# Kernel optimization log

Hardware: AMD Instinct MI355X
Metric: run time of the kernel (lower is better)

Reference implementation:

```python
import jax, jax.numpy as jnp
import numpy as np

VOCAB = 267735
CUTOFFS = [0, 20000, 40000, 200000, 267735]
D_EMBED = 1024
D_PROJ = 1024
DIV_VAL = 4
EMB_SCALE = float(D_PROJ) ** 0.5


def setup_inputs() -> dict:
    key = jax.random.key(0)
    ks = jax.random.split(key, 9)
    input_ids = jax.random.randint(ks[0], (8, 2048), 0, VOCAB, dtype=jnp.int64)
    inp = {"input_ids": input_ids}
    for i in range(4):
        l, r = CUTOFFS[i], CUTOFFS[i + 1]
        d_i = D_EMBED // (DIV_VAL ** i)
        inp[f"emb{i}"] = jax.random.normal(ks[1 + 2 * i], (r - l, d_i), dtype=jnp.float32) * 0.02
        inp[f"proj{i}"] = jax.random.normal(ks[2 + 2 * i], (D_PROJ, d_i), dtype=jnp.float32) * 0.02
    return inp


def reference(input_ids, emb0, emb1, emb2, emb3, proj0, proj1, proj2, proj3):
    tables = [emb0, emb1, emb2, emb3]
    projs = [proj0, proj1, proj2, proj3]
    out = jnp.zeros(input_ids.shape + (D_PROJ,), dtype=jnp.float32)
    for i in range(4):
        l, r = CUTOFFS[i], CUTOFFS[i + 1]
        mask = (input_ids >= l) & (input_ids < r)                     # [B,S]
        idx = jnp.clip(input_ids - l, 0, r - l - 1)                   # [B,S]
        emb_i = tables[i][idx]                                        # [B,S,d_i]
        proj_i = jnp.einsum('bse,de->bsd', emb_i, projs[i])           # [B,S,D]
        out = out + jnp.where(mask[..., None], proj_i, 0.0)
    return out * EMB_SCALE
```

## Files before the change

### kernel.cpp

```cpp
#include <hip/hip_runtime.h>


constexpr int NTOK  = 16384;
constexpr int DPROJ = 1024;
constexpr float EMB_SCALE = 32.0f;
constexpr int SLOTX = 264;

typedef __attribute__((ext_vector_type(8))) short short8;
typedef __attribute__((ext_vector_type(4))) float float4v;

__global__ __launch_bounds__(256) void partition_kernel(
    const int* __restrict__ ids, int* __restrict__ cnt, int* __restrict__ lists)
{
    int t = blockIdx.x * 256 + threadIdx.x;
    int id = ids[t];
    int c = (id >= 200000) ? 3 : (id >= 40000) ? 2 : (id >= 20000) ? 1 : 0;
    int lane = threadIdx.x & 63;
    unsigned long long lt = (1ull << lane) - 1ull;
    int pos = 0;
#pragma unroll
    for (int i = 0; i < 4; ++i) {
        unsigned long long m = __ballot(c == i);
        int b = 0;
        if (lane == 0 && m) b = atomicAdd(&cnt[i], (int)__popcll(m));
        b = __shfl(b, 0);
        if (c == i) pos = b + (int)__popcll(m & lt);
    }
    lists[c * NTOK + pos] = t;
}

__device__ __forceinline__ void gload_lds16(const float* g, void* l) {
    __builtin_amdgcn_global_load_lds(
        (const __attribute__((address_space(1))) void*)g,
        (__attribute__((address_space(3))) void*)l, 16, 0, 0);
}

__device__ __forceinline__ short f2bf(float f) {
    unsigned u = __builtin_bit_cast(unsigned, f);
    u += 0x7FFFu + ((u >> 16) & 1u);
    return (short)(u >> 16);
}

__device__ __forceinline__ short8 cvt8f(float4 a, float4 b) {
    short8 r = { f2bf(a.x), f2bf(a.y), f2bf(a.z), f2bf(a.w),
                 f2bf(b.x), f2bf(b.y), f2bf(b.z), f2bf(b.w) };
    return r;
}

template<int D, int NC>
__device__ __forceinline__ void gemm_pipe(
    const int* __restrict__ ids, const float* __restrict__ emb,
    const float* __restrict__ proj, const int* __restrict__ list,
    int count, int lo, int mtile, int n0,
    float* __restrict__ out, char* smem, int* smTok, int* smRow)
{
    const int m0 = mtile * 64;
    if (m0 >= count) return;
    const int tid = threadIdx.x, lane = tid & 63, wv = tid >> 6;
    const int col = lane & 15, quad = lane >> 4;
    const int wr = (wv >> 1) * 32, wc = (wv & 1) * 32;

    if (tid < 64) {
        int m = m0 + tid;
        int tok = (m < count) ? list[m] : -1;
        smTok[tid] = tok;
        smRow[tid] = (tok >= 0) ? (ids[tok] - lo) : 0;
    }
    __syncthreads();

    float (*As)[2048] = (float(*)[2048])smem;
    float (*Bs)[2048] = (float(*)[2048])(smem + 2 * 8192);

    const float* srcA[2]; const float* srcB[2]; int LL[2];
#pragma unroll
    for (int i = 0; i < 2; ++i) {
        int L = i * 4096 + wv * 1024 + lane * 16;
        int row = L >> 7;
        int kblk = ((L >> 4) & 7) ^ (row & 7);
        LL[i] = L;
        srcA[i] = emb  + (size_t)smRow[row] * D + kblk * 4;
        srcB[i] = proj + (size_t)(n0 + row) * D + kblk * 4;
    }

    auto issue = [&](int c, int buf) {
        const int co = c * 32;
#pragma unroll
        for (int i = 0; i < 2; ++i) gload_lds16(srcA[i] + co, (char*)As[buf] + LL[i]);
#pragma unroll
        for (int i = 0; i < 2; ++i) gload_lds16(srcB[i] + co, (char*)Bs[buf] + LL[i]);
    };

    float4v acc[2][2] = {};
    auto compute = [&](int buf) {
        short8 af[2], bf[2];
#pragma unroll
        for (int m = 0; m < 2; ++m) {
            int row = wr + m * 16 + col;
            const float* Ab = As[buf] + row * 32;
            float4 x = *(const float4*)(Ab + (((2 * quad + 0) ^ (row & 7)) << 2));
            float4 y = *(const float4*)(Ab + (((2 * quad + 1) ^ (row & 7)) << 2));
            af[m] = cvt8f(x, y);
        }
#pragma unroll
        for (int n = 0; n < 2; ++n) {
            int row = wc + n * 16 + col;
            const float* Bb = Bs[buf] + row * 32;
            float4 x = *(const float4*)(Bb + (((2 * quad + 0) ^ (row & 7)) << 2));
            float4 y = *(const float4*)(Bb + (((2 * quad + 1) ^ (row & 7)) << 2));
            bf[n] = cvt8f(x, y);
        }
#pragma unroll
        for (int m = 0; m < 2; ++m)
#pragma unroll
            for (int n = 0; n < 2; ++n)
                acc[m][n] = __builtin_amdgcn_mfma_f32_16x16x32_bf16(
                    af[m], bf[n], acc[m][n], 0, 0, 0);
    };

    issue(0, 0);
    __syncthreads();
#pragma unroll
    for (int k = 0; k < NC; ++k) {
        if (k + 1 < NC) issue(k + 1, (k + 1) & 1);
        compute(k & 1);
        __syncthreads();
    }

#pragma unroll
    for (int m = 0; m < 2; ++m) {
#pragma unroll
        for (int r = 0; r < 4; ++r) {
            int tok = smTok[wr + m * 16 + quad * 4 + r];
            if (tok < 0) continue;
            float* op = out + (size_t)tok * DPROJ + n0 + wc + col;
            op[0]  = acc[m][0][r] * EMB_SCALE;
            op[16] = acc[m][1][r] * EMB_SCALE;
        }
    }
}

__device__ __forceinline__ void gemm_c3(
    const int* __restrict__ ids, const float* __restrict__ emb,
    const float* __restrict__ proj, const int* __restrict__ list,
    int count, int mtile, int n0,
    float* __restrict__ out, char* smem, int* smTok, int* smRow)
{
    const int m0 = mtile * 64;
    if (m0 >= count) return;
    const int tid = threadIdx.x, lane = tid & 63, wv = tid >> 6;
    const int col = lane & 15, quad = lane >> 4;
    const int wr = (wv >> 1) * 32, wc = (wv & 1) * 32;
    short (*Asm)[24] = (short(*)[24])smem;
    short (*Bsm)[24] = (short(*)[24])(smem + 64 * 24 * 2);

    if (tid < 64) {
        int m = m0 + tid;
        int tok = (m < count) ? list[m] : -1;
        smTok[tid] = tok;
        smRow[tid] = (tok >= 0) ? (ids[tok] - 200000) : 0;
    }
    __syncthreads();

    if (tid < 128) {
        int r = tid >> 1, c0 = (tid & 1) * 8;
        const float* p = emb + (size_t)smRow[r] * 16 + c0;
        float4 x = *(const float4*)p, y = *(const float4*)(p + 4);
        *(short8*)&Asm[r][c0] = cvt8f(x, y);
    } else {
        int t = tid - 128, r = t >> 1, c0 = (t & 1) * 8;
        const float* p = proj + (size_t)(n0 + r) * 16 + c0;
        float4 x = *(const float4*)p, y = *(const float4*)(p + 4);
        *(short8*)&Bsm[r][c0] = cvt8f(x, y);
    }
    __syncthreads();

    short8 z8 = {};
    short8 af[2], bf[2];
#pragma unroll
    for (int m = 0; m < 2; ++m)
        af[m] = (quad < 2) ? *(const short8*)&Asm[wr + m * 16 + col][quad * 8] : z8;
#pragma unroll
    for (int n = 0; n < 2; ++n)
        bf[n] = (quad < 2) ? *(const short8*)&Bsm[wc + n * 16 + col][quad * 8] : z8;

    float4v acc[2][2] = {};
#pragma unroll
    for (int m = 0; m < 2; ++m)
#pragma unroll
        for (int n = 0; n < 2; ++n)
            acc[m][n] = __builtin_amdgcn_mfma_f32_16x16x32_bf16(
                af[m], bf[n], acc[m][n], 0, 0, 0);

#pragma unroll
    for (int m = 0; m < 2; ++m) {
#pragma unroll
        for (int r = 0; r < 4; ++r) {
            int tok = smTok[wr + m * 16 + quad * 4 + r];
            if (tok < 0) continue;
            float* op = out + (size_t)tok * DPROJ + n0 + wc + col;
            op[0]  = acc[m][0][r] * EMB_SCALE;
            op[16] = acc[m][1][r] * EMB_SCALE;
        }
    }
}

__global__ __launch_bounds__(256) void adaptive_emb_gemm(
    const int* __restrict__ ids,
    const float* __restrict__ e0, const float* __restrict__ p0,
    const float* __restrict__ e1, const float* __restrict__ p1,
    const float* __restrict__ e2, const float* __restrict__ p2,
    const float* __restrict__ e3, const float* __restrict__ p3,
    const int* __restrict__ cnt, const int* __restrict__ lists,
    float* __restrict__ out)
{
    __shared__ __align__(16) char smem[32768];
    __shared__ int smTok[64], smRow[64];

    const int n0 = blockIdx.y * 64;
    int c0t = (cnt[0] + 63) >> 6;
    int c1t = (cnt[1] + 63) >> 6;
    int c2t = (cnt[2] + 63) >> 6;
    int c3t = (cnt[3] + 63) >> 6;
    int s = blockIdx.x;
    if (s < c0t) {
        gemm_pipe<1024, 32>(ids, e0, p0, lists, cnt[0], 0,
                            s, n0, out, smem, smTok, smRow);
        return;
    }
    s -= c0t;
    if (s < c1t) {
        gemm_pipe<256, 8>(ids, e1, p1, lists + NTOK, cnt[1], 20000,
                          s, n0, out, smem, smTok, smRow);
        return;
    }
    s -= c1t;
    if (s < c2t) {
        gemm_pipe<64, 2>(ids, e2, p2, lists + 2 * NTOK, cnt[2], 40000,
                         s, n0, out, smem, smTok, smRow);
        return;
    }
    s -= c2t;
    if (s < c3t)
        gemm_c3(ids, e3, p3, lists + 3 * NTOK, cnt[3], s, n0, out, smem, smTok, smRow);
}

extern "C" void kernel_launch(void* const* d_in, const int* in_sizes, int n_in,
                              void* d_out, int out_size, void* d_ws, size_t ws_size,
                              hipStream_t stream) {
    const int*   ids = (const int*)d_in[0];
    const float* e0  = (const float*)d_in[1];
    const float* p0  = (const float*)d_in[2];
    const float* e1  = (const float*)d_in[3];
    const float* p1  = (const float*)d_in[4];
    const float* e2  = (const float*)d_in[5];
    const float* p2  = (const float*)d_in[6];
    const float* e3  = (const float*)d_in[7];
    const float* p3  = (const float*)d_in[8];
    float* out = (float*)d_out;

    int* cnt   = (int*)d_ws;
    int* lists = cnt + 4;

    (void)hipMemsetAsync(cnt, 0, 4 * sizeof(int), stream);
    partition_kernel<<<dim3(NTOK / 256), 256, 0, stream>>>(ids, cnt, lists);

    adaptive_emb_gemm<<<dim3(SLOTX, DPROJ / 64), 256, 0, stream>>>(
        ids, e0, p0, e1, p1, e2, p2, e3, p3, cnt, lists, out);
}
```

Baseline: 235.1 us.

## Enlarge GEMM tiles to 128x128 and unify last cluster into pipelined path

Each block now covers a 128-token by 128-column tile instead of 64x64. Each wave computes all 128 rows against its own 32 columns, which raises reuse of the staged B tile and cuts the number of blocks and the redundant re-reads of the embedding and projection tiles. The dedicated cluster-3 kernel is removed in favour of a D=16 instance of the pipelined GEMM that zero-pads the unused K lanes. The cost is twice the LDS (64 KB per block), more accumulator registers, fewer blocks in flight, and token ids re-read from global memory in the epilogue.

```diff
diff --git a/kernel.cpp b/kernel.cpp
--- a/kernel.cpp
+++ b/kernel.cpp
@@ -4,7 +4,7 @@
 constexpr int NTOK  = 16384;
 constexpr int DPROJ = 1024;
 constexpr float EMB_SCALE = 32.0f;
-constexpr int SLOTX = 264;
+constexpr int SLOTX = 136;
 
 typedef __attribute__((ext_vector_type(8))) short short8;
 typedef __attribute__((ext_vector_type(4))) float float4v;
@@ -52,74 +52,80 @@
     const int* __restrict__ ids, const float* __restrict__ emb,
     const float* __restrict__ proj, const int* __restrict__ list,
     int count, int lo, int mtile, int n0,
-    float* __restrict__ out, char* smem, int* smTok, int* smRow)
+    float* __restrict__ out, char* smem)
 {
-    const int m0 = mtile * 64;
+    const int m0 = mtile * 128;
     if (m0 >= count) return;
     const int tid = threadIdx.x, lane = tid & 63, wv = tid >> 6;
     const int col = lane & 15, quad = lane >> 4;
-    const int wr = (wv >> 1) * 32, wc = (wv & 1) * 32;
-
-    if (tid < 64) {
+
+    int* tmp = (int*)smem;
+    if (tid < 128) {
         int m = m0 + tid;
-        int tok = (m < count) ? list[m] : -1;
-        smTok[tid] = tok;
-        smRow[tid] = (tok >= 0) ? (ids[tok] - lo) : 0;
+        int tok = (m < count) ? list[m] : 0;
+        tmp[tid] = (m < count) ? (ids[tok] - lo) : 0;
     }
     __syncthreads();
 
-    float (*As)[2048] = (float(*)[2048])smem;
-    float (*Bs)[2048] = (float(*)[2048])(smem + 2 * 8192);
-
-    const float* srcA[2]; const float* srcB[2]; int LL[2];
-#pragma unroll
-    for (int i = 0; i < 2; ++i) {
-        int L = i * 4096 + wv * 1024 + lane * 16;
+    int LL[4], rowA[4];
+#pragma unroll
+    for (int i = 0; i < 4; ++i) {
+        LL[i] = i * 4096 + wv * 1024 + lane * 16;
+        rowA[i] = tmp[LL[i] >> 7];
+    }
+    __syncthreads();
+
+    float (*As)[4096] = (float(*)[4096])smem;
+    float (*Bs)[4096] = (float(*)[4096])(smem + 2 * 16384);
+
+    const float* srcA[4]; const float* srcB[4];
+#pragma unroll
+    for (int i = 0; i < 4; ++i) {
+        int L = LL[i];
         int row = L >> 7;
-        int kblk = ((L >> 4) & 7) ^ (row & 7);
-        LL[i] = L;
-        srcA[i] = emb  + (size_t)smRow[row] * D + kblk * 4;
-        srcB[i] = proj + (size_t)(n0 + row) * D + kblk * 4;
+        int kb = ((L >> 4) & 7) ^ (row & 7);
+        int ka = (D >= 32 || kb * 4 < D) ? kb * 4 : 0;
+        srcA[i] = emb  + (size_t)rowA[i] * D + ka;
+        srcB[i] = proj + (size_t)(n0 + row) * D + ka;
     }
 
     auto issue = [&](int c, int buf) {
         const int co = c * 32;
 #pragma unroll
-        for (int i = 0; i < 2; ++i) gload_lds16(srcA[i] + co, (char*)As[buf] + LL[i]);
-#pragma unroll
-        for (int i = 0; i < 2; ++i) gload_lds16(srcB[i] + co, (char*)Bs[buf] + LL[i]);
+        for (int i = 0; i < 4; ++i) gload_lds16(srcA[i] + co, (char*)As[buf] + LL[i]);
+#pragma unroll
+        for (int i = 0; i < 4; ++i) gload_lds16(srcB[i] + co, (char*)Bs[buf] + LL[i]);
     };
 
-    float4v acc[2][2] = {};
+    float4v acc[8][2] = {};
     auto compute = [&](int buf) {
-        short8 af[2], bf[2];
-#pragma unroll
-        for (int m = 0; m < 2; ++m) {
-            int row = wr + m * 16 + col;
+        short8 bf[2];
+#pragma unroll
+        for (int n = 0; n < 2; ++n) {
+            int row = wv * 32 + n * 16 + col;
+            const float* Bb = Bs[buf] + row * 32;
+            float4 x = *(const float4*)(Bb + (((2 * quad + 0) ^ (row & 7)) << 2));
+            float4 y = *(const float4*)(Bb + (((2 * quad + 1) ^ (row & 7)) << 2));
+            if (D == 16 && quad >= 2) { x = float4{}; y = float4{}; }
+            bf[n] = cvt8f(x, y);
+        }
+#pragma unroll
+        for (int m = 0; m < 8; ++m) {
+            int row = m * 16 + col;
             const float* Ab = As[buf] + row * 32;
             float4 x = *(const float4*)(Ab + (((2 * quad + 0) ^ (row & 7)) << 2));
             float4 y = *(const float4*)(Ab + (((2 * quad + 1) ^ (row & 7)) << 2));
-            af[m] = cvt8f(x, y);
-        }
-#pragma unroll
-        for (int n = 0; n < 2; ++n) {
-            int row = wc + n * 16 + col;
-            const float* Bb = Bs[buf] + row * 32;
-            float4 x = *(const float4*)(Bb + (((2 * quad + 0) ^ (row & 7)) << 2));
-            float4 y = *(const float4*)(Bb + (((2 * quad + 1) ^ (row & 7)) << 2));
-            bf[n] = cvt8f(x, y);
-        }
-#pragma unroll
-        for (int m = 0; m < 2; ++m)
+            short8 af = cvt8f(x, y);
 #pragma unroll
             for (int n = 0; n < 2; ++n)
                 acc[m][n] = __builtin_amdgcn_mfma_f32_16x16x32_bf16(
-                    af[m], bf[n], acc[m][n], 0, 0, 0);
+                    af, bf[n], acc[m][n], 0, 0, 0);
+        }
     };
 
     issue(0, 0);
     __syncthreads();
-#pragma unroll
+#pragma unroll 2
     for (int k = 0; k < NC; ++k) {
         if (k + 1 < NC) issue(k + 1, (k + 1) & 1);
         compute(k & 1);
@@ -127,77 +133,13 @@
     }
 
 #pragma unroll
-    for (int m = 0; m < 2; ++m) {
+    for (int m = 0; m < 8; ++m) {
 #pragma unroll
         for (int r = 0; r < 4; ++r) {
-            int tok = smTok[wr + m * 16 + quad * 4 + r];
-            if (tok < 0) continue;
-            float* op = out + (size_t)tok * DPROJ + n0 + wc + col;
-            op[0]  = acc[m][0][r] * EMB_SCALE;
-            op[16] = acc[m][1][r] * EMB_SCALE;
-        }
-    }
-}
-
-__device__ __forceinline__ void gemm_c3(
-    const int* __restrict__ ids, const float* __restrict__ emb,
-    const float* __restrict__ proj, const int* __restrict__ list,
-    int count, int mtile, int n0,
-    float* __restrict__ out, char* smem, int* smTok, int* smRow)
-{
-    const int m0 = mtile * 64;
-    if (m0 >= count) return;
-    const int tid = threadIdx.x, lane = tid & 63, wv = tid >> 6;
-    const int col = lane & 15, quad = lane >> 4;
-    const int wr = (wv >> 1) * 32, wc = (wv & 1) * 32;
-    short (*Asm)[24] = (short(*)[24])smem;
-    short (*Bsm)[24] = (short(*)[24])(smem + 64 * 24 * 2);
-
-    if (tid < 64) {
-        int m = m0 + tid;
-        int tok = (m < count) ? list[m] : -1;
-        smTok[tid] = tok;
-        smRow[tid] = (tok >= 0) ? (ids[tok] - 200000) : 0;
-    }
-    __syncthreads();
-
-    if (tid < 128) {
-        int r = tid >> 1, c0 = (tid & 1) * 8;
-        const float* p = emb + (size_t)smRow[r] * 16 + c0;
-        float4 x = *(const float4*)p, y = *(const float4*)(p + 4);
-        *(short8*)&Asm[r][c0] = cvt8f(x, y);
-    } else {
-        int t = tid - 128, r = t >> 1, c0 = (t & 1) * 8;
-        const float* p = proj + (size_t)(n0 + r) * 16 + c0;
-        float4 x = *(const float4*)p, y = *(const float4*)(p + 4);
-        *(short8*)&Bsm[r][c0] = cvt8f(x, y);
-    }
-    __syncthreads();
-
-    short8 z8 = {};
-    short8 af[2], bf[2];
-#pragma unroll
-    for (int m = 0; m < 2; ++m)
-        af[m] = (quad < 2) ? *(const short8*)&Asm[wr + m * 16 + col][quad * 8] : z8;
-#pragma unroll
-    for (int n = 0; n < 2; ++n)
-        bf[n] = (quad < 2) ? *(const short8*)&Bsm[wc + n * 16 + col][quad * 8] : z8;
-
-    float4v acc[2][2] = {};
-#pragma unroll
-    for (int m = 0; m < 2; ++m)
-#pragma unroll
-        for (int n = 0; n < 2; ++n)
-            acc[m][n] = __builtin_amdgcn_mfma_f32_16x16x32_bf16(
-                af[m], bf[n], acc[m][n], 0, 0, 0);
-
-#pragma unroll
-    for (int m = 0; m < 2; ++m) {
-#pragma unroll
-        for (int r = 0; r < 4; ++r) {
-            int tok = smTok[wr + m * 16 + quad * 4 + r];
-            if (tok < 0) continue;
-            float* op = out + (size_t)tok * DPROJ + n0 + wc + col;
+            int mm = m * 16 + quad * 4 + r;
+            if (m0 + mm >= count) continue;
+            int tok = list[m0 + mm];
+            float* op = out + (size_t)tok * DPROJ + n0 + wv * 32 + col;
             op[0]  = acc[m][0][r] * EMB_SCALE;
             op[16] = acc[m][1][r] * EMB_SCALE;
         }
@@ -213,35 +155,31 @@
     const int* __restrict__ cnt, const int* __restrict__ lists,
     float* __restrict__ out)
 {
-    __shared__ __align__(16) char smem[32768];
-    __shared__ int smTok[64], smRow[64];
-
-    const int n0 = blockIdx.y * 64;
-    int c0t = (cnt[0] + 63) >> 6;
-    int c1t = (cnt[1] + 63) >> 6;
-    int c2t = (cnt[2] + 63) >> 6;
-    int c3t = (cnt[3] + 63) >> 6;
+    __shared__ __align__(16) char smem[65536];
+
+    const int n0 = blockIdx.y * 128;
+    int c0t = (cnt[0] + 127) >> 7;
+    int c1t = (cnt[1] + 127) >> 7;
+    int c2t = (cnt[2] + 127) >> 7;
+    int c3t = (cnt[3] + 127) >> 7;
     int s = blockIdx.x;
     if (s < c0t) {
-        gemm_pipe<1024, 32>(ids, e0, p0, lists, cnt[0], 0,
-                            s, n0, out, smem, smTok, smRow);
+        gemm_pipe<1024, 32>(ids, e0, p0, lists, cnt[0], 0, s, n0, out, smem);
         return;
     }
     s -= c0t;
     if (s < c1t) {
-        gemm_pipe<256, 8>(ids, e1, p1, lists + NTOK, cnt[1], 20000,
-                          s, n0, out, smem, smTok, smRow);
+        gemm_pipe<256, 8>(ids, e1, p1, lists + NTOK, cnt[1], 20000, s, n0, out, smem);
         return;
     }
     s -= c1t;
     if (s < c2t) {
-        gemm_pipe<64, 2>(ids, e2, p2, lists + 2 * NTOK, cnt[2], 40000,
-                         s, n0, out, smem, smTok, smRow);
+        gemm_pipe<64, 2>(ids, e2, p2, lists + 2 * NTOK, cnt[2], 40000, s, n0, out, smem);
         return;
     }
     s -= c2t;
     if (s < c3t)
-        gemm_c3(ids, e3, p3, lists + 3 * NTOK, cnt[3], s, n0, out, smem, smTok, smRow);
+        gemm_pipe<16, 1>(ids, e3, p3, lists + 3 * NTOK, cnt[3], 200000, s, n0, out, smem);
 }
 
 extern "C" void kernel_launch(void* const* d_in, const int* in_sizes, int n_in,
@@ -264,6 +202,6 @@
     (void)hipMemsetAsync(cnt, 0, 4 * sizeof(int), stream);
     partition_kernel<<<dim3(NTOK / 256), 256, 0, stream>>>(ids, cnt, lists);
 
-    adaptive_emb_gemm<<<dim3(SLOTX, DPROJ / 64), 256, 0, stream>>>(
+    adaptive_emb_gemm<<<dim3(SLOTX, DPROJ / 128), 256, 0, stream>>>(
         ids, e0, p0, e1, p1, e2, p2, e3, p3, cnt, lists, out);
 }
```

Result: slower. 240.0 us (+2.1%).
